# Kernel optimization log

Hardware: AMD Instinct MI355X
Metric: run time of the kernel (lower is better)

Reference implementation:

```python
import jax, jax.numpy as jnp
import numpy as np

N, K = 1024, 128


def setup_inputs() -> dict:
    key = jax.random.key(0)
    k0, k1, k2, k3, k4 = jax.random.split(key, 5)
    beta = jax.random.uniform(k0, (N, N), dtype=jnp.float32)  # attention weights
    # omega must be invertible: small perturbation of identity, well-conditioned
    omega = jax.random.normal(k1, (N, K, K), dtype=jnp.float32) * 0.1 + jnp.eye(K, dtype=jnp.float32)
    # precisions are SPD in the physical model: A A^T / K + I
    A = jax.random.normal(k2, (N, K, K), dtype=jnp.float32)
    precision_p = jnp.einsum('nij,nkj->nik', A, A) / K + jnp.eye(K, dtype=jnp.float32)
    B = jax.random.normal(k3, (N, K, K), dtype=jnp.float32)
    precision_q = jnp.einsum('nij,nkj->nik', B, B) / K + jnp.eye(K, dtype=jnp.float32)
    C = jax.random.normal(k4, (K, K), dtype=jnp.float32)
    obs_precision = C @ C.T / K + jnp.eye(K, dtype=jnp.float32)
    return {
        'beta': beta,
        'omega': omega,
        'precision_p': precision_p,
        'precision_q': precision_q,
        'obs_precision': obs_precision,
    }


def reference(beta, omega, precision_p, precision_q, obs_precision):
    """Vectorized effective_mass_diagonal (Eq. 37).

    M_i = Lp_i + sum_{k!=i} beta_ik * Om_ik^{-T} Lq_k Om_ik^{-1}
               + (sum_{j!=i} beta_ji) * Lq_i + obs_precision
    with Om_ik = Om_i Om_k^{-1}, so Om_ik^{-1} = Om_k Om_i^{-1} and the
    sandwiched term factors as Om_i^{-T} (sum_k beta_ik * Om_k^T Lq_k Om_k) Om_i^{-1},
    turning the O(N^2) tiny-inverse loop into batched GEMMs + N inverses.
    """
    n = beta.shape[0]
    eye_mask = 1.0 - jnp.eye(n, dtype=beta.dtype)
    beta_nd = beta * eye_mask  # zero diagonal (k==i and j==i skipped)

    omega_inv = jnp.linalg.inv(omega)  # (N,K,K), batched
    # S_k = Omega_k^T Lq_k Omega_k, shape (N,K,K)
    S = jnp.einsum('nji,njk,nkl->nil', omega, precision_q, omega)
    # weighted accumulation over k != i: (N,N) x (N,K,K) -> (N,K,K)
    W = jnp.einsum('ik,kab->iab', beta_nd, S)
    # sandwich with Omega_i^{-T} ... Omega_i^{-1}
    cross = jnp.einsum('nji,njk,nkl->nil', omega_inv, W, omega_inv)

    col_sum = beta_nd.sum(axis=0)  # sum_j beta_ji, shape (N,)
    M = precision_p + cross + col_sum[:, None, None] * precision_q + obs_precision[None, :, :]
    return M  # (N, K, K)
```

## Files before the change

### kernel.cpp

```cpp
#include <hip/hip_runtime.h>

#define NN 1024
#define KK 128

typedef __attribute__((ext_vector_type(8))) short bf16x8;
typedef __attribute__((ext_vector_type(4))) float f32x4;
typedef __attribute__((ext_vector_type(8))) unsigned short u16x8;

__device__ __forceinline__ unsigned int bf16rne(float x) {
    unsigned int u = __float_as_uint(x);
    return (u + 0x7FFFu + ((u >> 16) & 1u)) >> 16;
}

__device__ __forceinline__ void split8(const float* xs, bf16x8& h8, bf16x8& l8) {
    #pragma unroll
    for (int j = 0; j < 8; ++j) {
        unsigned int hb = bf16rne(xs[j]);
        float hf = __uint_as_float(hb << 16);
        h8[j] = (short)hb;
        l8[j] = (short)bf16rne(xs[j] - hf);
    }
}

template<bool FINAL>
__global__ __launch_bounds__(512) void sandwich_mfma(
    const float* __restrict__ A_, const float* __restrict__ B_,
    float* __restrict__ Out,
    const float* __restrict__ Lp, const float* __restrict__ Lq,
    const float* __restrict__ obs, const float* __restrict__ beta)
{
    __shared__ short lds_buf[69632];
    short* Bth = lds_buf;
    short* Btl = lds_buf + 17408;
    short* Tth = lds_buf + 34816;
    short* Ttl = lds_buf + 52224;
    float* pan = (float*)(lds_buf + 34816);
    __shared__ float wred[8];
    __shared__ float cs_sh;

    const int n    = blockIdx.x;
    const int tid  = threadIdx.x;
    const int lane = tid & 63;
    const int wid  = tid >> 6;
    const int wr   = wid >> 1;
    const int wc   = wid & 1;
    const int lm   = lane & 15;
    const int lk   = lane >> 4;
    const size_t base = (size_t)n * (KK * KK);

    if (FINAL) {
        float s = 0.f;
        for (int j = tid; j < NN; j += 512)
            if (j != n) s += beta[(size_t)j * NN + n];
        #pragma unroll
        for (int off = 32; off >= 1; off >>= 1) s += __shfl_down(s, off);
        if (lane == 0) wred[wid] = s;
        __syncthreads();
        if (tid == 0) {
            float t = 0.f;
            #pragma unroll
            for (int w = 0; w < 8; ++w) t += wred[w];
            cs_sh = t;
        }
    }

    #pragma unroll
    for (int cp = 0; cp < 2; ++cp) {
        #pragma unroll
        for (int it = 0; it < 4; ++it) {
            int gid = it * 512 + tid;
            int k   = gid >> 4;
            int c4  = (gid & 15) * 4;
            *(float4*)&pan[k * 66 + c4] =
                *(const float4*)(B_ + base + (size_t)k * KK + cp * 64 + c4);
        }
        __syncthreads();
        #pragma unroll
        for (int it = 0; it < 2; ++it) {
            int t  = it * 512 + tid;
            int c  = t >> 4;
            int ko = (t & 15) * 8;
            float xs[8];
            #pragma unroll
            for (int j = 0; j < 8; ++j) xs[j] = pan[(ko + j) * 66 + c];
            bf16x8 h8, l8;
            split8(xs, h8, l8);
            const int gc = cp * 64 + c;
            *(bf16x8*)&Bth[gc * 136 + ko] = h8;
            *(bf16x8*)&Btl[gc * 136 + ko] = l8;
        }
        __syncthreads();
    }

    f32x4 acc[2][4];
    #pragma unroll
    for (int a = 0; a < 2; ++a)
        #pragma unroll
        for (int b = 0; b < 4; ++b) acc[a][b] = (f32x4){0.f, 0.f, 0.f, 0.f};

    #pragma unroll 1
    for (int ks = 0; ks < 4; ++ks) {
        const int k0 = ks * 32;
        bf16x8 afh[2], afl[2], bfh[4], bfl[4];
        #pragma unroll
        for (int rt = 0; rt < 2; ++rt) {
            const int r = wr * 32 + rt * 16 + lm;
            const float* ap = A_ + base + (size_t)r * KK + k0 + lk * 8;
            float4 x0 = *(const float4*)ap;
            float4 x1 = *(const float4*)(ap + 4);
            float xs[8] = {x0.x, x0.y, x0.z, x0.w, x1.x, x1.y, x1.z, x1.w};
            split8(xs, afh[rt], afl[rt]);
        }
        #pragma unroll
        for (int ct = 0; ct < 4; ++ct) {
            const int c = wc * 64 + ct * 16 + lm;
            bfh[ct] = *(const bf16x8*)&Bth[c * 136 + k0 + lk * 8];
            bfl[ct] = *(const bf16x8*)&Btl[c * 136 + k0 + lk * 8];
        }
        #pragma unroll
        for (int rt = 0; rt < 2; ++rt)
            #pragma unroll
            for (int ct = 0; ct < 4; ++ct) {
                acc[rt][ct] = __builtin_amdgcn_mfma_f32_16x16x32_bf16(
                    afh[rt], bfh[ct], acc[rt][ct], 0, 0, 0);
                acc[rt][ct] = __builtin_amdgcn_mfma_f32_16x16x32_bf16(
                    afh[rt], bfl[ct], acc[rt][ct], 0, 0, 0);
                acc[rt][ct] = __builtin_amdgcn_mfma_f32_16x16x32_bf16(
                    afl[rt], bfh[ct], acc[rt][ct], 0, 0, 0);
            }
    }

    #pragma unroll
    for (int rt = 0; rt < 2; ++rt)
        #pragma unroll
        for (int ct = 0; ct < 4; ++ct) {
            const int col  = wc * 64 + ct * 16 + lm;
            const int row0 = wr * 32 + rt * 16 + lk * 4;
            unsigned short h[4], l[4];
            #pragma unroll
            for (int j = 0; j < 4; ++j) {
                float x = acc[rt][ct][j];
                unsigned int hb = bf16rne(x);
                h[j] = (unsigned short)hb;
                l[j] = (unsigned short)bf16rne(x - __uint_as_float(hb << 16));
            }
            *(ushort4*)&Tth[col * 136 + row0] = make_ushort4(h[0], h[1], h[2], h[3]);
            *(ushort4*)&Ttl[col * 136 + row0] = make_ushort4(l[0], l[1], l[2], l[3]);
        }
    __syncthreads();

    f32x4 acc2[2][4];
    #pragma unroll
    for (int a = 0; a < 2; ++a)
        #pragma unroll
        for (int b = 0; b < 4; ++b) acc2[a][b] = (f32x4){0.f, 0.f, 0.f, 0.f};

    #pragma unroll 1
    for (int ks = 0; ks < 4; ++ks) {
        const int k0 = ks * 32;
        bf16x8 afh[2], afl[2], bfh[4], bfl[4];
        #pragma unroll
        for (int rt = 0; rt < 2; ++rt) {
            const int r = wr * 32 + rt * 16 + lm;
            afh[rt] = *(const bf16x8*)&Bth[r * 136 + k0 + lk * 8];
            afl[rt] = *(const bf16x8*)&Btl[r * 136 + k0 + lk * 8];
        }
        #pragma unroll
        for (int ct = 0; ct < 4; ++ct) {
            const int c = wc * 64 + ct * 16 + lm;
            bfh[ct] = *(const bf16x8*)&Tth[c * 136 + k0 + lk * 8];
            bfl[ct] = *(const bf16x8*)&Ttl[c * 136 + k0 + lk * 8];
        }
        #pragma unroll
        for (int rt = 0; rt < 2; ++rt)
            #pragma unroll
            for (int ct = 0; ct < 4; ++ct) {
                acc2[rt][ct] = __builtin_amdgcn_mfma_f32_16x16x32_bf16(
                    afh[rt], bfh[ct], acc2[rt][ct], 0, 0, 0);
                acc2[rt][ct] = __builtin_amdgcn_mfma_f32_16x16x32_bf16(
                    afh[rt], bfl[ct], acc2[rt][ct], 0, 0, 0);
                acc2[rt][ct] = __builtin_amdgcn_mfma_f32_16x16x32_bf16(
                    afl[rt], bfh[ct], acc2[rt][ct], 0, 0, 0);
            }
    }

    const float csv = FINAL ? cs_sh : 0.f;
    #pragma unroll
    for (int rt = 0; rt < 2; ++rt)
        #pragma unroll
        for (int ct = 0; ct < 4; ++ct) {
            const int col  = wc * 64 + ct * 16 + lm;
            const int row0 = wr * 32 + rt * 16 + lk * 4;
            #pragma unroll
            for (int j = 0; j < 4; ++j) {
                const int row = row0 + j;
                float o = acc2[rt][ct][j];
                if (FINAL) {
                    o += Lp[base + (size_t)row * KK + col]
                       + csv * Lq[base + (size_t)row * KK + col]
                       + obs[(size_t)row * KK + col];
                }
                Out[base + (size_t)row * KK + col] = o;
            }
        }
}

__global__ __launch_bounds__(256) void split_transpose_kernel(
    const float* __restrict__ S,
    unsigned short* __restrict__ Th, unsigned short* __restrict__ Tl)
{
    __shared__ float tile[128][132];
    const int tid = threadIdx.x;
    const int c0  = blockIdx.x * 128;
    const int k0  = blockIdx.y * 128;

    #pragma unroll
    for (int it = 0; it < 16; ++it) {
        int gid = it * 256 + tid;
        int kk  = gid >> 5;
        int c4  = (gid & 31) * 4;
        float4 v = *(const float4*)(S + (size_t)(k0 + kk) * 16384 + c0 + c4);
        *(float4*)&tile[kk][c4] = v;
    }
    __syncthreads();
    #pragma unroll
    for (int it = 0; it < 8; ++it) {
        int gid = it * 256 + tid;
        int c   = gid >> 4;
        int kc  = (gid & 15) * 8;
        u16x8 h, l;
        #pragma unroll
        for (int j = 0; j < 8; ++j) {
            float x = tile[kc + j][c];
            unsigned int hb = bf16rne(x);
            float hf = __uint_as_float(hb << 16);
            h[j] = (unsigned short)hb;
            l[j] = (unsigned short)bf16rne(x - hf);
        }
        size_t o = (size_t)(c0 + c) * 1024 + k0 + kc;
        *(u16x8*)(Th + o) = h;
        *(u16x8*)(Tl + o) = l;
    }
}

__global__ __launch_bounds__(256) void beta_split_kernel(
    const float* __restrict__ beta,
    unsigned short* __restrict__ Bh, unsigned short* __restrict__ Bl)
{
    const int gid = blockIdx.x * 256 + threadIdx.x;
    const int r   = gid >> 8;
    const int c4  = (gid & 255) * 4;
    float4 v = *(const float4*)(beta + (size_t)r * NN + c4);
    if (r == c4 + 0) v.x = 0.f;
    if (r == c4 + 1) v.y = 0.f;
    if (r == c4 + 2) v.z = 0.f;
    if (r == c4 + 3) v.w = 0.f;
    float xs[4] = {v.x, v.y, v.z, v.w};
    unsigned short hs[4], ls[4];
    #pragma unroll
    for (int j = 0; j < 4; ++j) {
        unsigned int hb = bf16rne(xs[j]);
        hs[j] = (unsigned short)hb;
        ls[j] = (unsigned short)bf16rne(xs[j] - __uint_as_float(hb << 16));
    }
    *(ushort4*)(Bh + (size_t)r * NN + c4) = make_ushort4(hs[0], hs[1], hs[2], hs[3]);
    *(ushort4*)(Bl + (size_t)r * NN + c4) = make_ushort4(ls[0], ls[1], ls[2], ls[3]);
}

template<bool PRESPLIT>
__global__ __launch_bounds__(256) void gemm_beta_mfma(
    const float* __restrict__ beta,
    const unsigned short* __restrict__ Bth_g,
    const unsigned short* __restrict__ Btl_g,
    const unsigned short* __restrict__ Sth,
    const unsigned short* __restrict__ Stl,
    float* __restrict__ W)
{
    __shared__ unsigned short Ah[128][44], Al[128][44];
    __shared__ unsigned short Bh[128][44], Bl[128][44];

    const int tid  = threadIdx.x;
    const int lane = tid & 63;
    const int wid  = tid >> 6;
    const int wr   = wid >> 1, wc = wid & 1;
    const int lm   = lane & 15;
    const int lk   = lane >> 4;
    const int i0   = blockIdx.y * 128;
    const int cb   = blockIdx.x * 128;

    f32x4 acc[4][4];
    #pragma unroll
    for (int a = 0; a < 4; ++a)
        #pragma unroll
        for (int b = 0; b < 4; ++b) acc[a][b] = (f32x4){0.f, 0.f, 0.f, 0.f};

    for (int k0 = 0; k0 < 1024; k0 += 32) {
        if (PRESPLIT) {
            #pragma unroll
            for (int it = 0; it < 2; ++it) {
                int gid = it * 256 + tid;
                int r   = gid >> 2;
                int kc  = (gid & 3) * 8;
                size_t o = (size_t)(i0 + r) * NN + k0 + kc;
                *(u16x8*)&Ah[r][kc] = *(const u16x8*)(Bth_g + o);
                *(u16x8*)&Al[r][kc] = *(const u16x8*)(Btl_g + o);
            }
        } else {
            #pragma unroll
            for (int it = 0; it < 4; ++it) {
                int gid = it * 256 + tid;
                int r   = gid >> 3;
                int c4  = (gid & 7) * 4;
                int gi  = i0 + r;
                float4 v = *(const float4*)(beta + (size_t)gi * NN + k0 + c4);
                if (gi == k0 + c4 + 0) v.x = 0.f;
                if (gi == k0 + c4 + 1) v.y = 0.f;
                if (gi == k0 + c4 + 2) v.z = 0.f;
                if (gi == k0 + c4 + 3) v.w = 0.f;
                float xs[4] = {v.x, v.y, v.z, v.w};
                unsigned short hs[4], ls[4];
                #pragma unroll
                for (int j = 0; j < 4; ++j) {
                    unsigned int hb = bf16rne(xs[j]);
                    hs[j] = (unsigned short)hb;
                    ls[j] = (unsigned short)bf16rne(xs[j] - __uint_as_float(hb << 16));
                }
                *(ushort4*)&Ah[r][c4] = make_ushort4(hs[0], hs[1], hs[2], hs[3]);
                *(ushort4*)&Al[r][c4] = make_ushort4(ls[0], ls[1], ls[2], ls[3]);
            }
        }
        #pragma unroll
        for (int it = 0; it < 2; ++it) {
            int gid = it * 256 + tid;
            int c   = gid >> 2;
            int kc  = (gid & 3) * 8;
            size_t o = (size_t)(cb + c) * 1024 + k0 + kc;
            *(u16x8*)&Bh[c][kc] = *(const u16x8*)(Sth + o);
            *(u16x8*)&Bl[c][kc] = *(const u16x8*)(Stl + o);
        }
        __syncthreads();

        bf16x8 afh[4], afl[4], bfh[4], bfl[4];
        #pragma unroll
        for (int rt = 0; rt < 4; ++rt) {
            const int r = wr * 64 + rt * 16 + lm;
            afh[rt] = *(const bf16x8*)&Ah[r][lk * 8];
            afl[rt] = *(const bf16x8*)&Al[r][lk * 8];
        }
        #pragma unroll
        for (int ct = 0; ct < 4; ++ct) {
            const int c = wc * 64 + ct * 16 + lm;
            bfh[ct] = *(const bf16x8*)&Bh[c][lk * 8];
            bfl[ct] = *(const bf16x8*)&Bl[c][lk * 8];
        }
        #pragma unroll
        for (int rt = 0; rt < 4; ++rt)
            #pragma unroll
            for (int ct = 0; ct < 4; ++ct) {
                acc[rt][ct] = __builtin_amdgcn_mfma_f32_16x16x32_bf16(
                    afh[rt], bfh[ct], acc[rt][ct], 0, 0, 0);
                acc[rt][ct] = __builtin_amdgcn_mfma_f32_16x16x32_bf16(
                    afh[rt], bfl[ct], acc[rt][ct], 0, 0, 0);
                acc[rt][ct] = __builtin_amdgcn_mfma_f32_16x16x32_bf16(
                    afl[rt], bfh[ct], acc[rt][ct], 0, 0, 0);
            }
        __syncthreads();
    }

    #pragma unroll
    for (int rt = 0; rt < 4; ++rt)
        #pragma unroll
        for (int ct = 0; ct < 4; ++ct) {
            const int col = cb + wc * 64 + ct * 16 + lm;
            #pragma unroll
            for (int j = 0; j < 4; ++j) {
                const int row = i0 + wr * 64 + rt * 16 + lk * 4 + j;
                W[(size_t)row * 16384 + col] = acc[rt][ct][j];
            }
        }
}

__global__ __launch_bounds__(512) void invert_kernel(
    const float* __restrict__ Om, float* __restrict__ Inv)
{
    const int n   = blockIdx.x;
    const int tid = threadIdx.x;
    const int rg  = tid >> 4;
    const int cg  = tid & 15;
    const int r0  = rg * 4;
    const int c0  = cg * 8;
    const size_t base = (size_t)n * (KK * KK);

    float4 a4[4][2];
    #pragma unroll
    for (int i = 0; i < 4; ++i) {
        const float* src = Om + base + (size_t)(r0 + i) * KK + c0;
        a4[i][0] = *(const float4*)(src);
        a4[i][1] = *(const float4*)(src + 4);
    }

    __shared__ __align__(16) float rowblk[2][4][132];
    __shared__ __align__(16) float rowstar[2][4][132];
    __shared__ __align__(16) float cpan[2][128][4];

    for (int g = 0; g < 32; ++g) {
        const int buf = g & 1;
        const int pgc = g >> 1;
        const int sub = g & 1;

        if (rg == g) {
            #pragma unroll
            for (int p = 0; p < 4; ++p) {
                *(float4*)&rowblk[buf][p][c0]     = a4[p][0];
                *(float4*)&rowblk[buf][p][c0 + 4] = a4[p][1];
            }
        }
        if (cg == pgc) {
            if (sub == 0) {
                #pragma unroll
                for (int i = 0; i < 4; ++i)
                    *(float4*)&cpan[buf][r0 + i][0] = a4[i][0];
            } else {
                #pragma unroll
                for (int i = 0; i < 4; ++i)
                    *(float4*)&cpan[buf][r0 + i][0] = a4[i][1];
            }
        }
        __syncthreads();

        float4 p0 = *(const float4*)&rowblk[buf][0][4 * g];
        float4 p1 = *(const float4*)&rowblk[buf][1][4 * g];
        float4 p2 = *(const float4*)&rowblk[buf][2][4 * g];
        float4 p3 = *(const float4*)&rowblk[buf][3][4 * g];
        const float s0 = p0.x*p1.y - p1.x*p0.y;
        const float s1 = p0.x*p1.z - p1.x*p0.z;
        const float s2 = p0.x*p1.w - p1.x*p0.w;
        const float s3 = p0.y*p1.z - p1.y*p0.z;
        const float s4 = p0.y*p1.w - p1.y*p0.w;
        const float s5 = p0.z*p1.w - p1.z*p0.w;
        const float c5 = p2.z*p3.w - p3.z*p2.w;
        const float c4 = p2.y*p3.w - p3.y*p2.w;
        const float c3 = p2.y*p3.z - p3.y*p2.z;
        const float c2 = p2.x*p3.w - p3.x*p2.w;
        const float c1 = p2.x*p3.z - p3.x*p2.z;
        const float c0f = p2.x*p3.y - p3.x*p2.y;
        const float det = s0*c5 - s1*c4 + s2*c3 + s3*c2 - s4*c1 + s5*c0f;
        const float id  = 1.0f / det;

        {
            const int c = tid & 127;
            const float r0v = rowblk[buf][0][c];
            const float r1v = rowblk[buf][1][c];
            const float r2v = rowblk[buf][2][c];
            const float r3v = rowblk[buf][3][c];
            const int cl = c - 4 * g;
            const int pq = tid >> 7;
            if (pq == 0) {
                const float Pi0 = ( p1.y*c5 - p1.z*c4 + p1.w*c3) * id;
                const float Pi1 = (-p0.y*c5 + p0.z*c4 - p0.w*c3) * id;
                const float Pi2 = ( p3.y*s5 - p3.z*s4 + p3.w*s3) * id;
                const float Pi3 = (-p2.y*s5 + p2.z*s4 - p2.w*s3) * id;
                float v = Pi0*r0v + Pi1*r1v + Pi2*r2v + Pi3*r3v;
                if      (cl == 0) v += Pi0;
                else if (cl == 1) v += Pi1;
                else if (cl == 2) v += Pi2;
                else if (cl == 3) v += Pi3;
                rowstar[buf][0][c] = v;
            } else if (pq == 1) {
                const float Pi0 = (-p1.x*c5 + p1.z*c2 - p1.w*c1) * id;
                const float Pi1 = ( p0.x*c5 - p0.z*c2 + p0.w*c1) * id;
                const float Pi2 = (-p3.x*s5 + p3.z*s2 - p3.w*s1) * id;
                const float Pi3 = ( p2.x*s5 - p2.z*s2 + p2.w*s1) * id;
                float v = Pi0*r0v + Pi1*r1v + Pi2*r2v + Pi3*r3v;
                if      (cl == 0) v += Pi0;
                else if (cl == 1) v += Pi1;
                else if (cl == 2) v += Pi2;
                else if (cl == 3) v += Pi3;
                rowstar[buf][1][c] = v;
            } else if (pq == 2) {
                const float Pi0 = ( p1.x*c4 - p1.y*c2 + p1.w*c0f) * id;
                const float Pi1 = (-p0.x*c4 + p0.y*c2 - p0.w*c0f) * id;
                const float Pi2 = ( p3.x*s4 - p3.y*s2 + p3.w*s0) * id;
                const float Pi3 = (-p2.x*s4 + p2.y*s2 - p2.w*s0) * id;
                float v = Pi0*r0v + Pi1*r1v + Pi2*r2v + Pi3*r3v;
                if      (cl == 0) v += Pi0;
                else if (cl == 1) v += Pi1;
                else if (cl == 2) v += Pi2;
                else if (cl == 3) v += Pi3;
                rowstar[buf][2][c] = v;
            } else {
                const float Pi0 = (-p1.x*c3 + p1.y*c1 - p1.z*c0f) * id;
                const float Pi1 = ( p0.x*c3 - p0.y*c1 + p0.z*c0f) * id;
                const float Pi2 = (-p3.x*s3 + p3.y*s1 - p3.z*s0) * id;
                const float Pi3 = ( p2.x*s3 - p2.y*s1 + p2.z*s0) * id;
                float v = Pi0*r0v + Pi1*r1v + Pi2*r2v + Pi3*r3v;
                if      (cl == 0) v += Pi0;
                else if (cl == 1) v += Pi1;
                else if (cl == 2) v += Pi2;
                else if (cl == 3) v += Pi3;
                rowstar[buf][3][c] = v;
            }
        }
        __syncthreads();

        const bool piv_rg = (rg == g);
        #pragma unroll
        for (int h = 0; h < 2; ++h) {
            const int ch = c0 + h * 4;
            float4 rs0 = *(const float4*)&rowstar[buf][0][ch];
            float4 rs1 = *(const float4*)&rowstar[buf][1][ch];
            float4 rs2 = *(const float4*)&rowstar[buf][2][ch];
            float4 rs3 = *(const float4*)&rowstar[buf][3][ch];
            #pragma unroll
            for (int i = 0; i < 4; ++i) {
                float4 f = *(const float4*)&cpan[buf][r0 + i][0];
                if (piv_rg) {
                    if (i == 0) f.x -= 1.0f;
                    else if (i == 1) f.y -= 1.0f;
                    else if (i == 2) f.z -= 1.0f;
                    else f.w -= 1.0f;
                }
                a4[i][h].x = fmaf(-f.x, rs0.x, fmaf(-f.y, rs1.x, fmaf(-f.z, rs2.x, fmaf(-f.w, rs3.x, a4[i][h].x))));
                a4[i][h].y = fmaf(-f.x, rs0.y, fmaf(-f.y, rs1.y, fmaf(-f.z, rs2.y, fmaf(-f.w, rs3.y, a4[i][h].y))));
                a4[i][h].z = fmaf(-f.x, rs0.z, fmaf(-f.y, rs1.z, fmaf(-f.z, rs2.z, fmaf(-f.w, rs3.z, a4[i][h].z))));
                a4[i][h].w = fmaf(-f.x, rs0.w, fmaf(-f.y, rs1.w, fmaf(-f.z, rs2.w, fmaf(-f.w, rs3.w, a4[i][h].w))));
            }
        }
    }

    #pragma unroll
    for (int i = 0; i < 4; ++i) {
        float* dst = Inv + base + (size_t)(r0 + i) * KK + c0;
        *(float4*)(dst)     = a4[i][0];
        *(float4*)(dst + 4) = a4[i][1];
    }
}

extern "C" void kernel_launch(void* const* d_in, const int* in_sizes, int n_in,
                              void* d_out, int out_size, void* d_ws, size_t ws_size,
                              hipStream_t stream)
{
    const float* beta  = (const float*)d_in[0];
    const float* omega = (const float*)d_in[1];
    const float* Lp    = (const float*)d_in[2];
    const float* Lq    = (const float*)d_in[3];
    const float* obs   = (const float*)d_in[4];
    float* out = (float*)d_out;

    const size_t MATE = (size_t)NN * KK * KK;

    if (ws_size >= 2 * MATE * sizeof(float)) {
        float* S = (float*)d_ws;
        unsigned short* Sth = (unsigned short*)((char*)d_ws + MATE * sizeof(float));
        unsigned short* Stl = Sth + MATE;
        unsigned short* Bh  = (unsigned short*)d_ws;
        unsigned short* Bl  = Bh + (size_t)NN * NN;
        float* Inv  = (float*)((char*)d_ws + 2 * (size_t)NN * NN * sizeof(unsigned short));
        float* Wbuf = out;

        sandwich_mfma<false><<<dim3(NN), dim3(512), 0, stream>>>(
            Lq, omega, S, nullptr, nullptr, nullptr, nullptr);
        split_transpose_kernel<<<dim3(128, 8), dim3(256), 0, stream>>>(S, Sth, Stl);
        beta_split_kernel<<<dim3(1024), dim3(256), 0, stream>>>(beta, Bh, Bl);
        gemm_beta_mfma<true><<<dim3(128, 8), dim3(256), 0, stream>>>(
            beta, Bh, Bl, Sth, Stl, Wbuf);
        invert_kernel<<<dim3(NN), dim3(512), 0, stream>>>(omega, Inv);
        sandwich_mfma<true><<<dim3(NN), dim3(512), 0, stream>>>(
            Wbuf, Inv, out, Lp, Lq, obs, beta);
    } else {
        float* S = (float*)d_ws;
        unsigned short* Sth = (unsigned short*)out;
        unsigned short* Stl = Sth + MATE;
        float* Wbuf = (float*)d_ws;
        float* Inv  = out;

        sandwich_mfma<false><<<dim3(NN), dim3(512), 0, stream>>>(
            Lq, omega, S, nullptr, nullptr, nullptr, nullptr);
        split_transpose_kernel<<<dim3(128, 8), dim3(256), 0, stream>>>(S, Sth, Stl);
        gemm_beta_mfma<false><<<dim3(128, 8), dim3(256), 0, stream>>>(
            beta, nullptr, nullptr, Sth, Stl, Wbuf);
        invert_kernel<<<dim3(NN), dim3(512), 0, stream>>>(omega, Inv);
        sandwich_mfma<true><<<dim3(NN), dim3(512), 0, stream>>>(
            Wbuf, Inv, out, Lp, Lq, obs, beta);
    }
}
```

Baseline: 422.5 us.

## Fuse batched matrix inversion into final sandwich kernel prologue

Removes the separate invert_kernel launch and instead performs the blocked Gauss-Jordan inversion of each omega matrix inside the FINAL sandwich_mfma block. The result goes straight from registers into the bf16 hi/lo transposed LDS tiles, with no global round trip. This avoids writing and re-reading a 64 MB inverse buffer and one kernel launch. The cost is serial inversion work that now sits in front of the MFMA phase of the final kernel, plus scalar, likely bank-conflicted LDS stores for the transpose.

```diff
diff --git a/kernel.cpp b/kernel.cpp
--- a/kernel.cpp
+++ b/kernel.cpp
@@ -35,6 +35,9 @@
     short* Tth = lds_buf + 34816;
     short* Ttl = lds_buf + 52224;
     float* pan = (float*)(lds_buf + 34816);
+    float* rowblk_  = (float*)(lds_buf + 34816);
+    float* rowstar_ = rowblk_ + 1056;
+    float* cpan_    = rowstar_ + 1056;
     __shared__ float wred[8];
     __shared__ float cs_sh;
 
@@ -64,30 +67,192 @@
         }
     }
 
-    #pragma unroll
-    for (int cp = 0; cp < 2; ++cp) {
-        #pragma unroll
-        for (int it = 0; it < 4; ++it) {
-            int gid = it * 512 + tid;
-            int k   = gid >> 4;
-            int c4  = (gid & 15) * 4;
-            *(float4*)&pan[k * 66 + c4] =
-                *(const float4*)(B_ + base + (size_t)k * KK + cp * 64 + c4);
+    if constexpr (!FINAL) {
+        #pragma unroll
+        for (int cp = 0; cp < 2; ++cp) {
+            #pragma unroll
+            for (int it = 0; it < 4; ++it) {
+                int gid = it * 512 + tid;
+                int k   = gid >> 4;
+                int c4  = (gid & 15) * 4;
+                *(float4*)&pan[k * 66 + c4] =
+                    *(const float4*)(B_ + base + (size_t)k * KK + cp * 64 + c4);
+            }
+            __syncthreads();
+            #pragma unroll
+            for (int it = 0; it < 2; ++it) {
+                int t  = it * 512 + tid;
+                int c  = t >> 4;
+                int ko = (t & 15) * 8;
+                float xs[8];
+                #pragma unroll
+                for (int j = 0; j < 8; ++j) xs[j] = pan[(ko + j) * 66 + c];
+                bf16x8 h8, l8;
+                split8(xs, h8, l8);
+                const int gc = cp * 64 + c;
+                *(bf16x8*)&Bth[gc * 136 + ko] = h8;
+                *(bf16x8*)&Btl[gc * 136 + ko] = l8;
+            }
+            __syncthreads();
+        }
+    } else {
+        const int rg = tid >> 4;
+        const int cg = tid & 15;
+        const int r0 = rg * 4;
+        const int c0 = cg * 8;
+
+        float4 a4[4][2];
+        #pragma unroll
+        for (int i = 0; i < 4; ++i) {
+            const float* src = B_ + base + (size_t)(r0 + i) * KK + c0;
+            a4[i][0] = *(const float4*)(src);
+            a4[i][1] = *(const float4*)(src + 4);
+        }
+
+        for (int g = 0; g < 32; ++g) {
+            const int buf = g & 1;
+            const int pgc = g >> 1;
+            const int sub = g & 1;
+            float* RB = rowblk_ + buf * 528;
+            float* RS = rowstar_ + buf * 528;
+            float* CP = cpan_ + buf * 512;
+
+            if (rg == g) {
+                #pragma unroll
+                for (int p = 0; p < 4; ++p) {
+                    *(float4*)&RB[p * 132 + c0]     = a4[p][0];
+                    *(float4*)&RB[p * 132 + c0 + 4] = a4[p][1];
+                }
+            }
+            if (cg == pgc) {
+                if (sub == 0) {
+                    #pragma unroll
+                    for (int i = 0; i < 4; ++i)
+                        *(float4*)&CP[(r0 + i) * 4] = a4[i][0];
+                } else {
+                    #pragma unroll
+                    for (int i = 0; i < 4; ++i)
+                        *(float4*)&CP[(r0 + i) * 4] = a4[i][1];
+                }
+            }
+            __syncthreads();
+
+            float4 p0 = *(const float4*)&RB[0 * 132 + 4 * g];
+            float4 p1 = *(const float4*)&RB[1 * 132 + 4 * g];
+            float4 p2 = *(const float4*)&RB[2 * 132 + 4 * g];
+            float4 p3 = *(const float4*)&RB[3 * 132 + 4 * g];
+            const float s0 = p0.x*p1.y - p1.x*p0.y;
+            const float s1 = p0.x*p1.z - p1.x*p0.z;
+            const float s2 = p0.x*p1.w - p1.x*p0.w;
+            const float s3 = p0.y*p1.z - p1.y*p0.z;
+            const float s4 = p0.y*p1.w - p1.y*p0.w;
+            const float s5 = p0.z*p1.w - p1.z*p0.w;
+            const float c5 = p2.z*p3.w - p3.z*p2.w;
+            const float c4 = p2.y*p3.w - p3.y*p2.w;
+            const float c3 = p2.y*p3.z - p3.y*p2.z;
+            const float c2 = p2.x*p3.w - p3.x*p2.w;
+            const float c1 = p2.x*p3.z - p3.x*p2.z;
+            const float c0f = p2.x*p3.y - p3.x*p2.y;
+            const float det = s0*c5 - s1*c4 + s2*c3 + s3*c2 - s4*c1 + s5*c0f;
+            const float id  = 1.0f / det;
+
+            {
+                const int c = tid & 127;
+                const float r0v = RB[0 * 132 + c];
+                const float r1v = RB[1 * 132 + c];
+                const float r2v = RB[2 * 132 + c];
+                const float r3v = RB[3 * 132 + c];
+                const int cl = c - 4 * g;
+                const int pq = tid >> 7;
+                if (pq == 0) {
+                    const float Pi0 = ( p1.y*c5 - p1.z*c4 + p1.w*c3) * id;
+                    const float Pi1 = (-p0.y*c5 + p0.z*c4 - p0.w*c3) * id;
+                    const float Pi2 = ( p3.y*s5 - p3.z*s4 + p3.w*s3) * id;
+                    const float Pi3 = (-p2.y*s5 + p2.z*s4 - p2.w*s3) * id;
+                    float v = Pi0*r0v + Pi1*r1v + Pi2*r2v + Pi3*r3v;
+                    if      (cl == 0) v += Pi0;
+                    else if (cl == 1) v += Pi1;
+                    else if (cl == 2) v += Pi2;
+                    else if (cl == 3) v += Pi3;
+                    RS[0 * 132 + c] = v;
+                } else if (pq == 1) {
+                    const float Pi0 = (-p1.x*c5 + p1.z*c2 - p1.w*c1) * id;
+                    const float Pi1 = ( p0.x*c5 - p0.z*c2 + p0.w*c1) * id;
+                    const float Pi2 = (-p3.x*s5 + p3.z*s2 - p3.w*s1) * id;
+                    const float Pi3 = ( p2.x*s5 - p2.z*s2 + p2.w*s1) * id;
+                    float v = Pi0*r0v + Pi1*r1v + Pi2*r2v + Pi3*r3v;
+                    if      (cl == 0) v += Pi0;
+                    else if (cl == 1) v += Pi1;
+                    else if (cl == 2) v += Pi2;
+                    else if (cl == 3) v += Pi3;
+                    RS[1 * 132 + c] = v;
+                } else if (pq == 2) {
+                    const float Pi0 = ( p1.x*c4 - p1.y*c2 + p1.w*c0f) * id;
+                    const float Pi1 = (-p0.x*c4 + p0.y*c2 - p0.w*c0f) * id;
+                    const float Pi2 = ( p3.x*s4 - p3.y*s2 + p3.w*s0) * id;
+                    const float Pi3 = (-p2.x*s4 + p2.y*s2 - p2.w*s0) * id;
+                    float v = Pi0*r0v + Pi1*r1v + Pi2*r2v + Pi3*r3v;
+                    if      (cl == 0) v += Pi0;
+                    else if (cl == 1) v += Pi1;
+                    else if (cl == 2) v += Pi2;
+                    else if (cl == 3) v += Pi3;
+                    RS[2 * 132 + c] = v;
+                } else {
+                    const float Pi0 = (-p1.x*c3 + p1.y*c1 - p1.z*c0f) * id;
+                    const float Pi1 = ( p0.x*c3 - p0.y*c1 + p0.z*c0f) * id;
+                    const float Pi2 = (-p3.x*s3 + p3.y*s1 - p3.z*s0) * id;
+                    const float Pi3 = ( p2.x*s3 - p2.y*s1 + p2.z*s0) * id;
+                    float v = Pi0*r0v + Pi1*r1v + Pi2*r2v + Pi3*r3v;
+                    if      (cl == 0) v += Pi0;
+                    else if (cl == 1) v += Pi1;
+                    else if (cl == 2) v += Pi2;
+                    else if (cl == 3) v += Pi3;
+                    RS[3 * 132 + c] = v;
+                }
+            }
+            __syncthreads();
+
+            const bool piv_rg = (rg == g);
+            #pragma unroll
+            for (int h = 0; h < 2; ++h) {
+                const int ch = c0 + h * 4;
+                float4 rs0 = *(const float4*)&RS[0 * 132 + ch];
+                float4 rs1 = *(const float4*)&RS[1 * 132 + ch];
+                float4 rs2 = *(const float4*)&RS[2 * 132 + ch];
+                float4 rs3 = *(const float4*)&RS[3 * 132 + ch];
+                #pragma unroll
+                for (int i = 0; i < 4; ++i) {
+                    float4 f = *(const float4*)&CP[(r0 + i) * 4];
+                    if (piv_rg) {
+                        if (i == 0) f.x -= 1.0f;
+                        else if (i == 1) f.y -= 1.0f;
+                        else if (i == 2) f.z -= 1.0f;
+                        else f.w -= 1.0f;
+                    }
+                    a4[i][h].x = fmaf(-f.x, rs0.x, fmaf(-f.y, rs1.x, fmaf(-f.z, rs2.x, fmaf(-f.w, rs3.x, a4[i][h].x))));
+                    a4[i][h].y = fmaf(-f.x, rs0.y, fmaf(-f.y, rs1.y, fmaf(-f.z, rs2.y, fmaf(-f.w, rs3.y, a4[i][h].y))));
+                    a4[i][h].z = fmaf(-f.x, rs0.z, fmaf(-f.y, rs1.z, fmaf(-f.z, rs2.z, fmaf(-f.w, rs3.z, a4[i][h].z))));
+                    a4[i][h].w = fmaf(-f.x, rs0.w, fmaf(-f.y, rs1.w, fmaf(-f.z, rs2.w, fmaf(-f.w, rs3.w, a4[i][h].w))));
+                }
+            }
         }
         __syncthreads();
-        #pragma unroll
-        for (int it = 0; it < 2; ++it) {
-            int t  = it * 512 + tid;
-            int c  = t >> 4;
-            int ko = (t & 15) * 8;
-            float xs[8];
-            #pragma unroll
-            for (int j = 0; j < 8; ++j) xs[j] = pan[(ko + j) * 66 + c];
-            bf16x8 h8, l8;
-            split8(xs, h8, l8);
-            const int gc = cp * 64 + c;
-            *(bf16x8*)&Bth[gc * 136 + ko] = h8;
-            *(bf16x8*)&Btl[gc * 136 + ko] = l8;
+
+        #pragma unroll
+        for (int i = 0; i < 4; ++i) {
+            const int row = r0 + i;
+            #pragma unroll
+            for (int h = 0; h < 2; ++h) {
+                float xs[4] = {a4[i][h].x, a4[i][h].y, a4[i][h].z, a4[i][h].w};
+                #pragma unroll
+                for (int j = 0; j < 4; ++j) {
+                    const int col = c0 + h * 4 + j;
+                    unsigned int hb = bf16rne(xs[j]);
+                    Bth[col * 136 + row] = (short)hb;
+                    Btl[col * 136 + row] =
+                        (short)bf16rne(xs[j] - __uint_as_float(hb << 16));
+                }
+            }
         }
         __syncthreads();
     }
@@ -380,162 +545,6 @@
         }
 }
 
-__global__ __launch_bounds__(512) void invert_kernel(
-    const float* __restrict__ Om, float* __restrict__ Inv)
-{
-    const int n   = blockIdx.x;
-    const int tid = threadIdx.x;
-    const int rg  = tid >> 4;
-    const int cg  = tid & 15;
-    const int r0  = rg * 4;
-    const int c0  = cg * 8;
-    const size_t base = (size_t)n * (KK * KK);
-
-    float4 a4[4][2];
-    #pragma unroll
-    for (int i = 0; i < 4; ++i) {
-        const float* src = Om + base + (size_t)(r0 + i) * KK + c0;
-        a4[i][0] = *(const float4*)(src);
-        a4[i][1] = *(const float4*)(src + 4);
-    }
-
-    __shared__ __align__(16) float rowblk[2][4][132];
-    __shared__ __align__(16) float rowstar[2][4][132];
-    __shared__ __align__(16) float cpan[2][128][4];
-
-    for (int g = 0; g < 32; ++g) {
-        const int buf = g & 1;
-        const int pgc = g >> 1;
-        const int sub = g & 1;
-
-        if (rg == g) {
-            #pragma unroll
-            for (int p = 0; p < 4; ++p) {
-                *(float4*)&rowblk[buf][p][c0]     = a4[p][0];
-                *(float4*)&rowblk[buf][p][c0 + 4] = a4[p][1];
-            }
-        }
-        if (cg == pgc) {
-            if (sub == 0) {
-                #pragma unroll
-                for (int i = 0; i < 4; ++i)
-                    *(float4*)&cpan[buf][r0 + i][0] = a4[i][0];
-            } else {
-                #pragma unroll
-                for (int i = 0; i < 4; ++i)
-                    *(float4*)&cpan[buf][r0 + i][0] = a4[i][1];
-            }
-        }
-        __syncthreads();
-
-        float4 p0 = *(const float4*)&rowblk[buf][0][4 * g];
-        float4 p1 = *(const float4*)&rowblk[buf][1][4 * g];
-        float4 p2 = *(const float4*)&rowblk[buf][2][4 * g];
-        float4 p3 = *(const float4*)&rowblk[buf][3][4 * g];
-        const float s0 = p0.x*p1.y - p1.x*p0.y;
-        const float s1 = p0.x*p1.z - p1.x*p0.z;
-        const float s2 = p0.x*p1.w - p1.x*p0.w;
-        const float s3 = p0.y*p1.z - p1.y*p0.z;
-        const float s4 = p0.y*p1.w - p1.y*p0.w;
-        const float s5 = p0.z*p1.w - p1.z*p0.w;
-        const float c5 = p2.z*p3.w - p3.z*p2.w;
-        const float c4 = p2.y*p3.w - p3.y*p2.w;
-        const float c3 = p2.y*p3.z - p3.y*p2.z;
-        const float c2 = p2.x*p3.w - p3.x*p2.w;
-        const float c1 = p2.x*p3.z - p3.x*p2.z;
-        const float c0f = p2.x*p3.y - p3.x*p2.y;
-        const float det = s0*c5 - s1*c4 + s2*c3 + s3*c2 - s4*c1 + s5*c0f;
-        const float id  = 1.0f / det;
-
-        {
-            const int c = tid & 127;
-            const float r0v = rowblk[buf][0][c];
-            const float r1v = rowblk[buf][1][c];
-            const float r2v = rowblk[buf][2][c];
-            const float r3v = rowblk[buf][3][c];
-            const int cl = c - 4 * g;
-            const int pq = tid >> 7;
-            if (pq == 0) {
-                const float Pi0 = ( p1.y*c5 - p1.z*c4 + p1.w*c3) * id;
-                const float Pi1 = (-p0.y*c5 + p0.z*c4 - p0.w*c3) * id;
-                const float Pi2 = ( p3.y*s5 - p3.z*s4 + p3.w*s3) * id;
-                const float Pi3 = (-p2.y*s5 + p2.z*s4 - p2.w*s3) * id;
-                float v = Pi0*r0v + Pi1*r1v + Pi2*r2v + Pi3*r3v;
-                if      (cl == 0) v += Pi0;
-                else if (cl == 1) v += Pi1;
-                else if (cl == 2) v += Pi2;
-                else if (cl == 3) v += Pi3;
-                rowstar[buf][0][c] = v;
-            } else if (pq == 1) {
-                const float Pi0 = (-p1.x*c5 + p1.z*c2 - p1.w*c1) * id;
-                const float Pi1 = ( p0.x*c5 - p0.z*c2 + p0.w*c1) * id;
-                const float Pi2 = (-p3.x*s5 + p3.z*s2 - p3.w*s1) * id;
-                const float Pi3 = ( p2.x*s5 - p2.z*s2 + p2.w*s1) * id;
-                float v = Pi0*r0v + Pi1*r1v + Pi2*r2v + Pi3*r3v;
-                if      (cl == 0) v += Pi0;
-                else if (cl == 1) v += Pi1;
-                else if (cl == 2) v += Pi2;
-                else if (cl == 3) v += Pi3;
-                rowstar[buf][1][c] = v;
-            } else if (pq == 2) {
-                const float Pi0 = ( p1.x*c4 - p1.y*c2 + p1.w*c0f) * id;
-                const float Pi1 = (-p0.x*c4 + p0.y*c2 - p0.w*c0f) * id;
-                const float Pi2 = ( p3.x*s4 - p3.y*s2 + p3.w*s0) * id;
-                const float Pi3 = (-p2.x*s4 + p2.y*s2 - p2.w*s0) * id;
-                float v = Pi0*r0v + Pi1*r1v + Pi2*r2v + Pi3*r3v;
-                if      (cl == 0) v += Pi0;
-                else if (cl == 1) v += Pi1;
-                else if (cl == 2) v += Pi2;
-                else if (cl == 3) v += Pi3;
-                rowstar[buf][2][c] = v;
-            } else {
-                const float Pi0 = (-p1.x*c3 + p1.y*c1 - p1.z*c0f) * id;
-                const float Pi1 = ( p0.x*c3 - p0.y*c1 + p0.z*c0f) * id;
-                const float Pi2 = (-p3.x*s3 + p3.y*s1 - p3.z*s0) * id;
-                const float Pi3 = ( p2.x*s3 - p2.y*s1 + p2.z*s0) * id;
-                float v = Pi0*r0v + Pi1*r1v + Pi2*r2v + Pi3*r3v;
-                if      (cl == 0) v += Pi0;
-                else if (cl == 1) v += Pi1;
-                else if (cl == 2) v += Pi2;
-                else if (cl == 3) v += Pi3;
-                rowstar[buf][3][c] = v;
-            }
-        }
-        __syncthreads();
-
-        const bool piv_rg = (rg == g);
-        #pragma unroll
-        for (int h = 0; h < 2; ++h) {
-            const int ch = c0 + h * 4;
-            float4 rs0 = *(const float4*)&rowstar[buf][0][ch];
-            float4 rs1 = *(const float4*)&rowstar[buf][1][ch];
-            float4 rs2 = *(const float4*)&rowstar[buf][2][ch];
-            float4 rs3 = *(const float4*)&rowstar[buf][3][ch];
-            #pragma unroll
-            for (int i = 0; i < 4; ++i) {
-                float4 f = *(const float4*)&cpan[buf][r0 + i][0];
-                if (piv_rg) {
-                    if (i == 0) f.x -= 1.0f;
-                    else if (i == 1) f.y -= 1.0f;
-                    else if (i == 2) f.z -= 1.0f;
-                    else f.w -= 1.0f;
-                }
-                a4[i][h].x = fmaf(-f.x, rs0.x, fmaf(-f.y, rs1.x, fmaf(-f.z, rs2.x, fmaf(-f.w, rs3.x, a4[i][h].x))));
-                a4[i][h].y = fmaf(-f.x, rs0.y, fmaf(-f.y, rs1.y, fmaf(-f.z, rs2.y, fmaf(-f.w, rs3.y, a4[i][h].y))));
-                a4[i][h].z = fmaf(-f.x, rs0.z, fmaf(-f.y, rs1.z, fmaf(-f.z, rs2.z, fmaf(-f.w, rs3.z, a4[i][h].z))));
-                a4[i][h].w = fmaf(-f.x, rs0.w, fmaf(-f.y, rs1.w, fmaf(-f.z, rs2.w, fmaf(-f.w, rs3.w, a4[i][h].w))));
-            }
-        }
-    }
-
-    #pragma unroll
-    for (int i = 0; i < 4; ++i) {
-        float* dst = Inv + base + (size_t)(r0 + i) * KK + c0;
-        *(float4*)(dst)     = a4[i][0];
-        *(float4*)(dst + 4) = a4[i][1];
-    }
-}
-
 extern "C" void kernel_launch(void* const* d_in, const int* in_sizes, int n_in,
                               void* d_out, int out_size, void* d_ws, size_t ws_size,
                               hipStream_t stream)
@@ -555,7 +564,6 @@
         unsigned short* Stl = Sth + MATE;
         unsigned short* Bh  = (unsigned short*)d_ws;
         unsigned short* Bl  = Bh + (size_t)NN * NN;
-        float* Inv  = (float*)((char*)d_ws + 2 * (size_t)NN * NN * sizeof(unsigned short));
         float* Wbuf = out;
 
         sandwich_mfma<false><<<dim3(NN), dim3(512), 0, stream>>>(
@@ -564,23 +572,20 @@
         beta_split_kernel<<<dim3(1024), dim3(256), 0, stream>>>(beta, Bh, Bl);
         gemm_beta_mfma<true><<<dim3(128, 8), dim3(256), 0, stream>>>(
             beta, Bh, Bl, Sth, Stl, Wbuf);
-        invert_kernel<<<dim3(NN), dim3(512), 0, stream>>>(omega, Inv);
         sandwich_mfma<true><<<dim3(NN), dim3(512), 0, stream>>>(
-            Wbuf, Inv, out, Lp, Lq, obs, beta);
+            Wbuf, omega, out, Lp, Lq, obs, beta);
     } else {
         float* S = (float*)d_ws;
         unsigned short* Sth = (unsigned short*)out;
         unsigned short* Stl = Sth + MATE;
         float* Wbuf = (float*)d_ws;
-        float* Inv  = out;
 
         sandwich_mfma<false><<<dim3(NN), dim3(512), 0, stream>>>(
             Lq, omega, S, nullptr, nullptr, nullptr, nullptr);
         split_transpose_kernel<<<dim3(128, 8), dim3(256), 0, stream>>>(S, Sth, Stl);
         gemm_beta_mfma<false><<<dim3(128, 8), dim3(256), 0, stream>>>(
             beta, nullptr, nullptr, Sth, Stl, Wbuf);
-        invert_kernel<<<dim3(NN), dim3(512), 0, stream>>>(omega, Inv);
         sandwich_mfma<true><<<dim3(NN), dim3(512), 0, stream>>>(
-            Wbuf, Inv, out, Lp, Lq, obs, beta);
-    }
-}
+            Wbuf, omega, out, Lp, Lq, obs, beta);
+    }
+}
```

New measurement: 451.2 us. 1.07x slower.
